# Kernel optimization log

Measured on AMD Instinct MI355X. Metric: run time of the kernel, lower is better.

## Reference

```python
import jax, jax.numpy as jnp
import numpy as np

B, S, D, H = 2, 2048, 1024, 16
DK = D // H


def setup_inputs() -> dict:
    key = jax.random.key(0)
    ks = jax.random.split(key, 8)
    std = 0.02
    inp = {
        "query": jax.random.normal(ks[0], (B, S, D), jnp.float32),
        "key": jax.random.normal(ks[1], (B, S, D), jnp.float32),
        "value": jax.random.normal(ks[2], (B, S, D), jnp.float32),
        # causal mask, 1 = attend, 0 = masked (matches masked_fill(mask==0, -1e9))
        "mask": jnp.broadcast_to(
            jnp.tril(jnp.ones((S, S), jnp.int32))[None, None], (B, 1, S, S)
        ),
        "wq_w": jax.random.normal(ks[3], (D, D), jnp.float32) * std,
        "wq_b": jnp.zeros((D,), jnp.float32),
        "wk_w": jax.random.normal(ks[4], (D, D), jnp.float32) * std,
        "wk_b": jnp.zeros((D,), jnp.float32),
        "wv_w": jax.random.normal(ks[5], (D, D), jnp.float32) * std,
        "wv_b": jnp.zeros((D,), jnp.float32),
        "wo_w": jax.random.normal(ks[6], (D, D), jnp.float32) * std,
        "wo_b": jnp.zeros((D,), jnp.float32),
    }
    return inp


def _split_heads(x, b):
    # [B, S, D] -> [B, H, S, DK]
    return x.reshape(b, -1, H, DK).transpose(0, 2, 1, 3)


def reference(query, key, value, mask, wq_w, wq_b, wk_w, wk_b, wv_w, wv_b, wo_w, wo_b):
    b = query.shape[0]
    q = _split_heads(query @ wq_w.T + wq_b, b)
    k = _split_heads(key @ wk_w.T + wk_b, b)
    v = _split_heads(value @ wv_w.T + wv_b, b)

    scale = 1.0 / np.sqrt(DK).astype(np.float32)
    scores = jnp.einsum("bhqd,bhkd->bhqk", q, k) * scale  # [B,H,Sq,Sk]
    scores = jnp.where(mask == 0, jnp.float32(-1e9), scores)
    attn = jax.nn.softmax(scores, axis=-1)  # dropout p=0 (eval)

    ctx = jnp.einsum("bhqk,bhkd->bhqd", attn, v)  # [B,H,Sq,DK]
    ctx = ctx.transpose(0, 2, 1, 3).reshape(b, -1, D)  # [B,Sq,D]
    out = ctx @ wo_w.T + wo_b
    return out, attn
```

## Files before the change

kernel.cpp:

```cpp
#include <hip/hip_runtime.h>
#include <hip/hip_bf16.h>

#define B_ 2
#define S_ 2048
#define D_ 1024
#define H_ 16
#define DK_ 64

typedef __attribute__((ext_vector_type(8))) short bf16x8;
typedef __attribute__((ext_vector_type(4))) float f32x4;

#define MFMA16(a, b, c) __builtin_amdgcn_mfma_f32_16x16x32_bf16((a), (b), (c), 0, 0, 0)

__device__ __forceinline__ unsigned short f2bf(float f) {
  __hip_bfloat16 h = __float2bfloat16(f);
  return *reinterpret_cast<unsigned short*>(&h);
}

__device__ __forceinline__ void gload_lds16(const void* g, void* l) {
  __builtin_amdgcn_global_load_lds((const __attribute__((address_space(1))) void*)g,
                                   (__attribute__((address_space(3))) void*)l, 16, 0, 0);
}

__global__ __launch_bounds__(256) void cvt_all(
    const float* __restrict__ s0, const float* __restrict__ s1, const float* __restrict__ s2,
    const float* __restrict__ s3, const float* __restrict__ s4, const float* __restrict__ s5,
    const float* __restrict__ s6,
    unsigned short* __restrict__ d0, unsigned short* __restrict__ d1,
    unsigned short* __restrict__ d2, unsigned short* __restrict__ d3,
    unsigned short* __restrict__ d4, unsigned short* __restrict__ d5,
    unsigned short* __restrict__ d6, int nbig, int nsmall) {
  const float* src; unsigned short* dst; int n4;
  switch (blockIdx.y) {
    case 0: src = s0; dst = d0; n4 = nbig; break;
    case 1: src = s1; dst = d1; n4 = nbig; break;
    case 2: src = s2; dst = d2; n4 = nbig; break;
    case 3: src = s3; dst = d3; n4 = nsmall; break;
    case 4: src = s4; dst = d4; n4 = nsmall; break;
    case 5: src = s5; dst = d5; n4 = nsmall; break;
    default: src = s6; dst = d6; n4 = nsmall; break;
  }
  int i = blockIdx.x * blockDim.x + threadIdx.x;
  int stride = gridDim.x * blockDim.x;
  for (; i < n4; i += stride) {
    float4 v = ((const float4*)src)[i];
    ushort4 o;
    o.x = f2bf(v.x); o.y = f2bf(v.y); o.z = f2bf(v.z); o.w = f2bf(v.w);
    ((ushort4*)dst)[i] = o;
  }
}

__device__ __forceinline__ void gemm_body(const unsigned short* __restrict__ A,
                                          const unsigned short* __restrict__ W,
                                          const float* __restrict__ bias,
                                          void* __restrict__ out,
                                          int mode, float scale, int tm, int tn) {
  __shared__ __align__(16) unsigned short lsA[2][128 * 32];
  __shared__ __align__(16) unsigned short lsB[2][128 * 32];
  const int K = 1024;
  const int tid = threadIdx.x;
  const int w = tid >> 6, l = tid & 63;
  const int wm = w >> 2, wn = w & 3;
  const int cl = l & 15, lg = l >> 4;

  f32x4 acc[4][2];
#pragma unroll
  for (int i = 0; i < 4; ++i)
#pragma unroll
    for (int j = 0; j < 2; ++j) acc[i][j] = (f32x4){0.f, 0.f, 0.f, 0.f};

  const int srow = w * 16 + (l >> 2);
  const int slog = (l & 3) ^ ((srow >> 1) & 3);
  const unsigned short* Abase = A + (size_t)(tm * 128 + srow) * K + slog * 8;
  const unsigned short* Wbase = W + (size_t)(tn * 128 + srow) * K + slog * 8;

  gload_lds16(Abase, lsA[0] + w * 512);
  gload_lds16(Wbase, lsB[0] + w * 512);
  __syncthreads();

  for (int ks = 0; ks < 32; ++ks) {
    const int cur = ks & 1;
    if (ks + 1 < 32) {
      gload_lds16(Abase + (ks + 1) * 32, lsA[cur ^ 1] + w * 512);
      gload_lds16(Wbase + (ks + 1) * 32, lsB[cur ^ 1] + w * 512);
    }
    bf16x8 af[4], bfr[2];
#pragma unroll
    for (int f = 0; f < 4; ++f) {
      int ar = wm * 64 + f * 16 + cl;
      int ph = lg ^ ((ar >> 1) & 3);
      af[f] = *(const bf16x8*)(lsA[cur] + ar * 32 + ph * 8);
    }
#pragma unroll
    for (int f = 0; f < 2; ++f) {
      int br = wn * 32 + f * 16 + cl;
      int ph = lg ^ ((br >> 1) & 3);
      bfr[f] = *(const bf16x8*)(lsB[cur] + br * 32 + ph * 8);
    }
#pragma unroll
    for (int i = 0; i < 4; ++i)
#pragma unroll
      for (int j = 0; j < 2; ++j) acc[i][j] = MFMA16(af[i], bfr[j], acc[i][j]);
    __syncthreads();
  }

#pragma unroll
  for (int i = 0; i < 4; ++i) {
#pragma unroll
    for (int j = 0; j < 2; ++j) {
#pragma unroll
      for (int r = 0; r < 4; ++r) {
        int mm = tm * 128 + wm * 64 + i * 16 + 4 * lg + r;
        int nn = tn * 128 + wn * 32 + j * 16 + cl;
        float v = (acc[i][j][r] + bias[nn]) * scale;
        if (mode == 2) {
          ((float*)out)[(size_t)mm * 1024 + nn] = v;
        } else {
          int bb = mm >> 11, s = mm & 2047, hh = nn >> 6, dk = nn & 63;
          size_t idx = (mode == 0)
                           ? ((((size_t)bb * H_ + hh) * S_ + s) * DK_ + dk)
                           : ((((size_t)bb * H_ + hh) * DK_ + dk) * S_ + s);
          ((unsigned short*)out)[idx] = f2bf(v);
        }
      }
    }
  }
}

#define QSCALE 0.18033688011112042f

__global__ __launch_bounds__(512) void gemm_qkv(
    const unsigned short* __restrict__ xq, const unsigned short* __restrict__ xk,
    const unsigned short* __restrict__ xv, const unsigned short* __restrict__ wq,
    const unsigned short* __restrict__ wk, const unsigned short* __restrict__ wv,
    const float* __restrict__ bq, const float* __restrict__ bk, const float* __restrict__ bv,
    unsigned short* __restrict__ oq, unsigned short* __restrict__ ok,
    unsigned short* __restrict__ ov) {
  const int z = blockIdx.z;
  const unsigned short* A = (z == 0) ? xq : (z == 1) ? xk : xv;
  const unsigned short* W = (z == 0) ? wq : (z == 1) ? wk : wv;
  const float* bias = (z == 0) ? bq : (z == 1) ? bk : bv;
  void* out = (z == 0) ? (void*)oq : (z == 1) ? (void*)ok : (void*)ov;
  gemm_body(A, W, bias, out, (z == 2) ? 1 : 0, (z == 0) ? QSCALE : 1.0f,
            blockIdx.x, blockIdx.y);
}

__global__ __launch_bounds__(512) void gemm_out(const unsigned short* __restrict__ A,
                                                const unsigned short* __restrict__ W,
                                                const float* __restrict__ bias,
                                                float* __restrict__ out) {
  gemm_body(A, W, bias, out, 2, 1.0f, blockIdx.x, blockIdx.y);
}

__global__ __launch_bounds__(256) void attn_fused(const unsigned short* __restrict__ qh,
                                                  const unsigned short* __restrict__ kh,
                                                  const unsigned short* __restrict__ vt,
                                                  float* __restrict__ attn,
                                                  unsigned short* __restrict__ ctxh) {
  __shared__ __align__(16) unsigned short kst[2][4096];
  __shared__ __align__(16) unsigned short vst[2][4096];
  __shared__ __align__(16) float pT[4][16 * 68];
  const int wgid = blockIdx.x;
  const int y = wgid >> 3;
  const int qt = 31 - (y >> 2);
  const int bh = (wgid & 7) * 4 + (y & 3);
  const int b = bh >> 4, h = bh & 15;
  const int w = threadIdx.x >> 6, l = threadIdx.x & 63;
  const int cl = l & 15, lg = l >> 4;
  const int qrb = qt * 64 + w * 16;
  const int qloc = w * 16 + cl;

  const unsigned short* kbh = kh + (size_t)bh * S_ * DK_;
  const unsigned short* vbh = vt + (size_t)bh * DK_ * S_;

  bf16x8 aq0, aq1;
  {
    const unsigned short* qp = qh + (size_t)bh * S_ * DK_ + (size_t)(qrb + cl) * DK_ + lg * 8;
    aq0 = *(const bf16x8*)qp;
    aq1 = *(const bf16x8*)(qp + 32);
  }

  const int sr0 = w * 16 + (l >> 3);
  const int sc = l & 7;
  auto stageKp = [&](int kt, unsigned short* dst) {
    const char* base = (const char*)kbh + (size_t)kt * 8192;
#pragma unroll
    for (int call = 0; call < 2; ++call) {
      int r = sr0 + call * 8;
      gload_lds16(base + r * 128 + ((sc ^ (r & 7)) << 4),
                  (char*)dst + w * 2048 + call * 1024);
    }
  };
  auto stageV = [&](int kt, int buf) {
    const char* base = (const char*)vbh + (size_t)kt * 128;
#pragma unroll
    for (int call = 0; call < 2; ++call) {
      int r = sr0 + call * 8;
      gload_lds16(base + (size_t)r * (S_ * 2) + ((sc ^ (r & 7)) << 4),
                  (char*)vst[buf] + w * 2048 + call * 1024);
    }
  };
  auto readKp = [&](const unsigned short* buf, bf16x8(&k0)[4], bf16x8(&k1)[4]) {
#pragma unroll
    for (int mt = 0; mt < 4; ++mt) {
      int r = mt * 16 + cl;
      const char* rb = (const char*)buf + r * 128;
      k0[mt] = *(const bf16x8*)(rb + ((lg ^ (r & 7)) << 4));
      k1[mt] = *(const bf16x8*)(rb + (((4 + lg) ^ (r & 7)) << 4));
    }
  };
  auto kring = [&](int i) -> unsigned short* { return (i & 2) ? vst[i & 1] : kst[i & 1]; };

  f32x4 lsv = (f32x4){0.f, 0.f, 0.f, 0.f};
  auto procA = [&](const unsigned short* buf, bool diag) {
    bf16x8 k0[4], k1[4];
    readKp(buf, k0, k1);
    f32x4 cc[4];
#pragma unroll
    for (int mt = 0; mt < 4; ++mt) {
      f32x4 c = (f32x4){0.f, 0.f, 0.f, 0.f};
      c = MFMA16(k0[mt], aq0, c);
      cc[mt] = MFMA16(k1[mt], aq1, c);
    }
#pragma unroll
    for (int mt = 0; mt < 4; ++mt)
#pragma unroll
      for (int r = 0; r < 4; ++r) {
        float e = exp2f(cc[mt][r]);
        if (diag && (mt * 16 + 4 * lg + r > qloc)) e = 0.f;
        lsv[r] += e;
      }
  };

  stageKp(0, kring(0));
  if (qt >= 1) stageKp(1, kring(1));
  __syncthreads();
  for (int t = 0; t <= qt; t += 2) {
    if (t + 2 <= qt) stageKp(t + 2, kring(t + 2));
    if (t + 3 <= qt) stageKp(t + 3, kring(t + 3));
    procA(kring(t), t == qt);
    if (t + 1 <= qt) procA(kring(t + 1), t + 1 == qt);
    __syncthreads();
  }
  float ls = (lsv[0] + lsv[1]) + (lsv[2] + lsv[3]);
  ls += __shfl_xor(ls, 16);
  ls += __shfl_xor(ls, 32);
  const float inv = 1.0f / ls;

  f32x4 pv[4];
#pragma unroll
  for (int i = 0; i < 4; ++i) pv[i] = (f32x4){0.f, 0.f, 0.f, 0.f};
  float* pTw = pT[w];
  float* asrow = attn + (size_t)bh * S_ * S_ + (size_t)(qrb + lg) * S_ + 4 * cl;

  stageKp(0, kst[0]);
  stageV(0, 0);
  __syncthreads();
  for (int t = 0; t <= qt; ++t) {
    const int cur = t & 1;
    if (t < qt) {
      stageKp(t + 1, kst[cur ^ 1]);
      stageV(t + 1, cur ^ 1);
    }
    bf16x8 k0[4], k1[4];
    readKp(kst[cur], k0, k1);
    f32x4 cc[4];
#pragma unroll
    for (int mt = 0; mt < 4; ++mt) {
      f32x4 c = (f32x4){0.f, 0.f, 0.f, 0.f};
      c = MFMA16(k0[mt], aq0, c);
      cc[mt] = MFMA16(k1[mt], aq1, c);
    }
    const bool diag = (t == qt);
#pragma unroll
    for (int mt = 0; mt < 4; ++mt) {
      f32x4 pf;
#pragma unroll
      for (int r = 0; r < 4; ++r) {
        float p = exp2f(cc[mt][r]) * inv;
        if (diag && (mt * 16 + 4 * lg + r > qloc)) p = 0.f;
        pf[r] = p;
      }
      *(f32x4*)(pTw + cl * 68 + mt * 16 + 4 * lg) = pf;
    }
#pragma unroll
    for (int j = 0; j < 4; ++j) {
      f32x4 v = *(const f32x4*)(pTw + (4 * j + lg) * 68 + 4 * cl);
      *(f32x4*)(asrow + (size_t)(4 * j) * S_ + t * 64) = v;
    }
#pragma unroll
    for (int c2 = 0; c2 < 2; ++c2) {
      f32x4 pa0 = *(const f32x4*)(pTw + cl * 68 + c2 * 32 + 8 * lg);
      f32x4 pa1 = *(const f32x4*)(pTw + cl * 68 + c2 * 32 + 8 * lg + 4);
      bf16x8 pa;
#pragma unroll
      for (int i = 0; i < 4; ++i) {
        pa[i] = (short)f2bf(pa0[i]);
        pa[4 + i] = (short)f2bf(pa1[i]);
      }
#pragma unroll
      for (int n2 = 0; n2 < 4; ++n2) {
        int r = n2 * 16 + cl;
        const char* rb = (const char*)vst[cur] + r * 128;
        bf16x8 vb = *(const bf16x8*)(rb + (((c2 * 4 + lg) ^ (r & 7)) << 4));
        pv[n2] = MFMA16(pa, vb, pv[n2]);
      }
    }
    __syncthreads();
  }

  {
    const f32x4 z = (f32x4){0.f, 0.f, 0.f, 0.f};
    for (int c = (qt + 1) * 64; c < S_; c += 64) {
#pragma unroll
      for (int j = 0; j < 4; ++j)
        *(f32x4*)(asrow + (size_t)(4 * j) * S_ + c) = z;
    }
  }

#pragma unroll
  for (int n2 = 0; n2 < 4; ++n2)
#pragma unroll
    for (int r = 0; r < 4; ++r)
      ctxh[((size_t)b * S_ + qrb + 4 * lg + r) * D_ + h * DK_ + n2 * 16 + cl] =
          f2bf(pv[n2][r]);
}

extern "C" void kernel_launch(void* const* d_in, const int* in_sizes, int n_in,
                              void* d_out, int out_size, void* d_ws, size_t ws_size,
                              hipStream_t stream) {
  const float* q  = (const float*)d_in[0];
  const float* k  = (const float*)d_in[1];
  const float* v  = (const float*)d_in[2];
  const float* wq = (const float*)d_in[4];
  const float* bq = (const float*)d_in[5];
  const float* wk = (const float*)d_in[6];
  const float* bk = (const float*)d_in[7];
  const float* wv = (const float*)d_in[8];
  const float* bv = (const float*)d_in[9];
  const float* wo = (const float*)d_in[10];
  const float* bo = (const float*)d_in[11];

  float* out  = (float*)d_out;
  float* attn = out + (size_t)B_ * S_ * D_;

  char* ws = (char*)d_ws;
  const size_t MB = 1024 * 1024;
  unsigned short* xq   = (unsigned short*)(ws + 0 * MB);
  unsigned short* xk   = (unsigned short*)(ws + 8 * MB);
  unsigned short* xv   = (unsigned short*)(ws + 16 * MB);
  unsigned short* wqb  = (unsigned short*)(ws + 24 * MB);
  unsigned short* wkb  = (unsigned short*)(ws + 26 * MB);
  unsigned short* wvb  = (unsigned short*)(ws + 28 * MB);
  unsigned short* wob  = (unsigned short*)(ws + 30 * MB);
  unsigned short* qhb  = (unsigned short*)(ws + 32 * MB);
  unsigned short* khb  = (unsigned short*)(ws + 40 * MB);
  unsigned short* vtb  = (unsigned short*)(ws + 48 * MB);
  unsigned short* ctxh = (unsigned short*)(ws + 56 * MB);

  const int NX4 = (B_ * S_ * D_) / 4;
  const int NW4 = (D_ * D_) / 4;
  cvt_all<<<dim3(256, 7), 256, 0, stream>>>(q, k, v, wq, wk, wv, wo,
                                            xq, xk, xv, wqb, wkb, wvb, wob, NX4, NW4);

  gemm_qkv<<<dim3(32, 8, 3), 512, 0, stream>>>(xq, xk, xv, wqb, wkb, wvb,
                                               bq, bk, bv, qhb, khb, vtb);

  attn_fused<<<dim3(1024), 256, 0, stream>>>(qhb, khb, vtb, attn, ctxh);

  gemm_out<<<dim3(32, 8), 512, 0, stream>>>(ctxh, wob, bo, out);
}
```

Measured before the change: 248.0 us.

## Move causal-mask zero fill of attn into extra blocks of the GEMM kernels

The zero writes for the masked upper-triangle of the attention output move out of the fused attention kernel. They now run in extra z-slices of the QKV projection and output projection launches: half the stripes during QKV, half during the output GEMM. The aim is to overlap this store traffic with the compute-bound GEMMs and shorten the attention kernel's tail. The fill blocks use the GEMM's 512-thread configuration with 64 rows × 8 threads, so only 512 of 1024 stripes fit per launch. Correctness relies on the stripe count and index mapping covering every masked region exactly once.

```diff
diff --git a/kernel.cpp b/kernel.cpp
--- a/kernel.cpp
+++ b/kernel.cpp
@@ -20,6 +20,17 @@
 __device__ __forceinline__ void gload_lds16(const void* g, void* l) {
   __builtin_amdgcn_global_load_lds((const __attribute__((address_space(1))) void*)g,
                                    (__attribute__((address_space(3))) void*)l, 16, 0, 0);
+}
+
+__device__ __forceinline__ void fill_stripe(float* __restrict__ attn, int stripe) {
+  const int bh = stripe >> 5, qt = stripe & 31;
+  const int c0 = (qt + 1) * 64;
+  if (c0 >= S_) return;
+  const int tid = threadIdx.x;
+  const int r = tid >> 3;
+  float* row = attn + (size_t)bh * S_ * S_ + (size_t)(qt * 64 + r) * S_;
+  const f32x4 z = (f32x4){0.f, 0.f, 0.f, 0.f};
+  for (int c = c0 + (tid & 7) * 4; c < S_; c += 32) *(f32x4*)(row + c) = z;
 }
 
 __global__ __launch_bounds__(256) void cvt_all(
@@ -135,8 +146,14 @@
     const unsigned short* __restrict__ wk, const unsigned short* __restrict__ wv,
     const float* __restrict__ bq, const float* __restrict__ bk, const float* __restrict__ bv,
     unsigned short* __restrict__ oq, unsigned short* __restrict__ ok,
-    unsigned short* __restrict__ ov) {
+    unsigned short* __restrict__ ov, float* __restrict__ attn) {
   const int z = blockIdx.z;
+  if (z == 3) {
+    const int bid = blockIdx.x + 32 * blockIdx.y;
+    fill_stripe(attn, 2 * bid);
+    fill_stripe(attn, 2 * bid + 1);
+    return;
+  }
   const unsigned short* A = (z == 0) ? xq : (z == 1) ? xk : xv;
   const unsigned short* W = (z == 0) ? wq : (z == 1) ? wk : wv;
   const float* bias = (z == 0) ? bq : (z == 1) ? bk : bv;
@@ -148,7 +165,14 @@
 __global__ __launch_bounds__(512) void gemm_out(const unsigned short* __restrict__ A,
                                                 const unsigned short* __restrict__ W,
                                                 const float* __restrict__ bias,
-                                                float* __restrict__ out) {
+                                                float* __restrict__ out,
+                                                float* __restrict__ attn) {
+  if (blockIdx.z == 1) {
+    const int bid = blockIdx.x + 32 * blockIdx.y;
+    fill_stripe(attn, 512 + 2 * bid);
+    fill_stripe(attn, 512 + 2 * bid + 1);
+    return;
+  }
   gemm_body(A, W, bias, out, 2, 1.0f, blockIdx.x, blockIdx.y);
 }
 
@@ -309,15 +333,6 @@
     __syncthreads();
   }
 
-  {
-    const f32x4 z = (f32x4){0.f, 0.f, 0.f, 0.f};
-    for (int c = (qt + 1) * 64; c < S_; c += 64) {
-#pragma unroll
-      for (int j = 0; j < 4; ++j)
-        *(f32x4*)(asrow + (size_t)(4 * j) * S_ + c) = z;
-    }
-  }
-
 #pragma unroll
   for (int n2 = 0; n2 < 4; ++n2)
 #pragma unroll
@@ -363,10 +378,10 @@
   cvt_all<<<dim3(256, 7), 256, 0, stream>>>(q, k, v, wq, wk, wv, wo,
                                             xq, xk, xv, wqb, wkb, wvb, wob, NX4, NW4);
 
-  gemm_qkv<<<dim3(32, 8, 3), 512, 0, stream>>>(xq, xk, xv, wqb, wkb, wvb,
-                                               bq, bk, bv, qhb, khb, vtb);
+  gemm_qkv<<<dim3(32, 8, 4), 512, 0, stream>>>(xq, xk, xv, wqb, wkb, wvb,
+                                               bq, bk, bv, qhb, khb, vtb, attn);
 
   attn_fused<<<dim3(1024), 256, 0, stream>>>(qhb, khb, vtb, attn, ctxh);
 
-  gemm_out<<<dim3(32, 8), 512, 0, stream>>>(ctxh, wob, bo, out);
-}
+  gemm_out<<<dim3(32, 8, 2), 512, 0, stream>>>(ctxh, wob, bo, out, attn);
+}
```

Measured after the change: 263.0 us. 1.06x slower.
